# Kernel optimization log

Hardware: AMD Instinct MI355X
Metric: run time of the kernel (lower is better)

Reference implementation:

```python
import jax, jax.numpy as jnp
import numpy as np

N_NODES = 50000


def _add_self_loops(edge_index, num_nodes):
    loop = jnp.arange(num_nodes, dtype=edge_index.dtype)
    src = jnp.concatenate([edge_index[0], loop])
    dst = jnp.concatenate([edge_index[1], loop])
    return src, dst


def _gcn_norm(src, dst, num_nodes, dtype):
    # symmetric normalization: deg^{-1/2}[src] * deg^{-1/2}[dst]
    deg = jax.ops.segment_sum(jnp.ones_like(dst, dtype=dtype), dst,
                              num_segments=num_nodes)
    dinv = jnp.where(deg > 0, jax.lax.rsqrt(deg), 0.0).astype(dtype)
    return dinv[src] * dinv[dst]


def _gcn_conv(x, src, dst, norm, W, b, num_nodes):
    h = x @ W                                  # [N, out]
    msg = norm[:, None] * h[src]               # [E', out] gather
    agg = jax.ops.segment_sum(msg, dst, num_segments=num_nodes)  # scatter-add
    return agg + b


def setup_inputs() -> dict:
    key = jax.random.key(0)
    k1, k2, k3, k4 = jax.random.split(key, 4)
    x = jax.random.normal(k1, (N_NODES, 64), dtype=jnp.float32)
    edge_index = jax.random.randint(k2, (2, 800000), 0, N_NODES, dtype=jnp.int64)
    W1 = jax.random.normal(k3, (64, 64), dtype=jnp.float32) * (1.0 / np.sqrt(64))
    b1 = jnp.zeros((64,), dtype=jnp.float32)
    W2 = jax.random.normal(k4, (64, 37), dtype=jnp.float32) * (1.0 / np.sqrt(64))
    b2 = jnp.zeros((37,), dtype=jnp.float32)
    return {"x": x, "edge_index": edge_index, "W1": W1, "b1": b1,
            "W2": W2, "b2": b2}


def reference(x, edge_index, W1, b1, W2, b2):
    n = x.shape[0]
    src, dst = _add_self_loops(edge_index, n)
    norm = _gcn_norm(src, dst, n, x.dtype)
    h = _gcn_conv(x, src, dst, norm, W1, b1, n)
    h = jax.nn.relu(h)
    out = _gcn_conv(h, src, dst, norm, W2, b2, n)
    return out
```

## Files before the change

### kernel.cpp

```cpp
#include <hip/hip_runtime.h>
#include <hip/hip_fp16.h>

#define F_OUT 37
#define BSHIFT 7
#define BSIZE 128
#define CAP 3072
#define STAGE_CAP 6144
#define XS_STRIDE 68

__device__ __forceinline__ short4 pack4(float a, float b, float c, float d) {
    union { __half2 h2[2]; short4 s; } u;
    u.h2[0] = __floats2half2_rn(a, b);
    u.h2[1] = __floats2half2_rn(c, d);
    return u.s;
}
__device__ __forceinline__ float4 unpack4(short4 v) {
    union { short4 s; __half2 h2[2]; } u;
    u.s = v;
    float2 lo = __half22float2(u.h2[0]);
    float2 hi = __half22float2(u.h2[1]);
    return make_float4(lo.x, lo.y, hi.x, hi.y);
}


__global__ __launch_bounds__(256) void bucketA(const int* __restrict__ src,
                                               const int* __restrict__ dst,
                                               int E, int C, int nb,
                                               int* __restrict__ gcur,
                                               unsigned* __restrict__ bedge) {
    __shared__ unsigned stage[STAGE_CAP];
    __shared__ int lcnt[400];
    __shared__ int lbase[400];
    int t = threadIdx.x;
    int e0 = blockIdx.x * C;
    int cnt = E - e0; if (cnt > C) cnt = C; if (cnt <= 0) return;

    for (int i = t; i < nb; i += 256) lcnt[i] = 0;
    __syncthreads();
    for (int i = t; i < cnt; i += 256) {
        int s = src[e0 + i], d = dst[e0 + i];
        int b = d >> BSHIFT;
        atomicAdd(&lcnt[b], 1);
        stage[i] = ((unsigned)b << 23) | ((unsigned)(d & (BSIZE - 1)) << 16) | (unsigned)s;
    }
    __syncthreads();
    for (int i = t; i < nb; i += 256)
        lbase[i] = lcnt[i] ? atomicAdd(&gcur[i * 16], lcnt[i]) : 0;
    __syncthreads();
    for (int i = t; i < nb; i += 256) lcnt[i] = 0;
    __syncthreads();
    for (int i = t; i < cnt; i += 256) {
        unsigned w = stage[i];
        int b = w >> 23;
        int pos = b * CAP + lbase[b] + atomicAdd(&lcnt[b], 1);
        bedge[pos] = w & 0x7FFFFFu;
    }
}

__global__ __launch_bounds__(256) void bucketB(const unsigned* __restrict__ bedge,
                                               const int* __restrict__ gcur,
                                               int n,
                                               int* __restrict__ rowbeg,
                                               int* __restrict__ rowend,
                                               int* __restrict__ srcIdx,
                                               float* __restrict__ dinv) {
    __shared__ int hcnt[BSIZE], hoff[BSIZE], hcur[BSIZE], tmp[BSIZE];
    int b = blockIdx.x;
    int t = threadIdx.x;
    int cntb = gcur[b * 16];
    int base = b * CAP;
    const unsigned* ed = bedge + (size_t)base;

    if (t < BSIZE) { hcnt[t] = 0; hcur[t] = 0; }
    __syncthreads();
    for (int i = t; i < cntb; i += 256) atomicAdd(&hcnt[ed[i] >> 16], 1);
    __syncthreads();
    if (t < BSIZE) tmp[t] = hcnt[t];
    __syncthreads();
    for (int o = 1; o < BSIZE; o <<= 1) {
        int a = (t < BSIZE && t >= o) ? tmp[t - o] : 0;
        __syncthreads();
        if (t < BSIZE) tmp[t] += a;
        __syncthreads();
    }
    if (t < BSIZE) hoff[t] = tmp[t] - hcnt[t];
    __syncthreads();
    int node = b * BSIZE + t;
    if (t < BSIZE && node < n) {
        rowbeg[node] = base + hoff[t];
        rowend[node] = base + hoff[t] + hcnt[t];
        dinv[node] = rsqrtf(1.0f + (float)hcnt[t]);
    }
    for (int i = t; i < cntb; i += 256) {
        unsigned w = ed[i];
        int dloc = w >> 16;
        int pos = base + hoff[dloc] + atomicAdd(&hcur[dloc], 1);
        srcIdx[pos] = (int)(w & 0xFFFFu);
    }
}


#define MICRO_STEP(XI, ACC)                                                    \
    do {                                                                       \
        ACC[0] += XI.x * w0.x; ACC[1] += XI.x * w0.y;                          \
        ACC[2] += XI.x * w0.z; ACC[3] += XI.x * w0.w;                          \
        ACC[0] += XI.y * w1.x; ACC[1] += XI.y * w1.y;                          \
        ACC[2] += XI.y * w1.z; ACC[3] += XI.y * w1.w;                          \
        ACC[0] += XI.z * w2.x; ACC[1] += XI.z * w2.y;                          \
        ACC[2] += XI.z * w2.z; ACC[3] += XI.z * w2.w;                          \
        ACC[0] += XI.w * w3.x; ACC[1] += XI.w * w3.y;                          \
        ACC[2] += XI.w * w3.z; ACC[3] += XI.w * w3.w;                          \
    } while (0)

__global__ __launch_bounds__(256, 4) void gemm64(const float* __restrict__ x,
                                                 const float* __restrict__ W,
                                                 const float* __restrict__ dinv,
                                                 short4* __restrict__ hsv, int n) {
    __shared__ float Xs[64 * XS_STRIDE];
    __shared__ float Ws[64 * 64];
    int t = threadIdx.x;
    const float4* W4 = (const float4*)W;
#pragma unroll
    for (int i = 0; i < 4; ++i)
        ((float4*)Ws)[t + i * 256] = W4[t + i * 256];
    int row0 = blockIdx.x * 64;
#pragma unroll
    for (int i = 0; i < 4; ++i) {
        int idx = i * 256 + t;
        int r = idx >> 4, k4 = idx & 15;
        int grow = row0 + r;
        float4 v = (grow < n) ? ((const float4*)x)[(size_t)grow * 16 + k4]
                              : make_float4(0.f, 0.f, 0.f, 0.f);
        *(float4*)&Xs[r * XS_STRIDE + k4 * 4] = v;
    }
    __syncthreads();

    int tc = t & 15, tr = t >> 4;
    float a0[4] = {0.f, 0.f, 0.f, 0.f};
    float a1[4] = {0.f, 0.f, 0.f, 0.f};
    float a2[4] = {0.f, 0.f, 0.f, 0.f};
    float a3[4] = {0.f, 0.f, 0.f, 0.f};

#pragma unroll 2
    for (int k = 0; k < 64; k += 4) {
        float4 w0 = *(const float4*)&Ws[(k + 0) * 64 + 4 * tc];
        float4 w1 = *(const float4*)&Ws[(k + 1) * 64 + 4 * tc];
        float4 w2 = *(const float4*)&Ws[(k + 2) * 64 + 4 * tc];
        float4 w3 = *(const float4*)&Ws[(k + 3) * 64 + 4 * tc];
        float4 x0 = *(const float4*)&Xs[(4 * tr + 0) * XS_STRIDE + k];
        float4 x1 = *(const float4*)&Xs[(4 * tr + 1) * XS_STRIDE + k];
        float4 x2 = *(const float4*)&Xs[(4 * tr + 2) * XS_STRIDE + k];
        float4 x3 = *(const float4*)&Xs[(4 * tr + 3) * XS_STRIDE + k];
        MICRO_STEP(x0, a0);
        MICRO_STEP(x1, a1);
        MICRO_STEP(x2, a2);
        MICRO_STEP(x3, a3);
    }

#define STORE64(ACC, R)                                                        \
    do {                                                                       \
        int row = row0 + 4 * tr + (R);                                         \
        if (row < n) {                                                         \
            float dd = dinv[row];                                              \
            hsv[(size_t)row * 16 + tc] =                                       \
                pack4(ACC[0] * dd, ACC[1] * dd, ACC[2] * dd, ACC[3] * dd);     \
        }                                                                      \
    } while (0)
    STORE64(a0, 0); STORE64(a1, 1); STORE64(a2, 2); STORE64(a3, 3);
#undef STORE64
}

__global__ __launch_bounds__(256, 4) void gemm37(const short4* __restrict__ h1v,
                                                 const float* __restrict__ W,
                                                 short4* __restrict__ g32v,
                                                 short4* __restrict__ g8v, int n) {
    __shared__ float Xs[64 * XS_STRIDE];
    __shared__ float Ws[64 * 64];
    int t = threadIdx.x;
    for (int i = t; i < 64 * 64; i += 256) {
        int k = i >> 6, c = i & 63;
        Ws[i] = (c < F_OUT) ? W[k * F_OUT + c] : 0.f;
    }
    int row0 = blockIdx.x * 64;
#pragma unroll
    for (int i = 0; i < 4; ++i) {
        int idx = i * 256 + t;
        int r = idx >> 4, k4 = idx & 15;
        int grow = row0 + r;
        float4 v = (grow < n) ? unpack4(h1v[(size_t)grow * 16 + k4])
                              : make_float4(0.f, 0.f, 0.f, 0.f);
        *(float4*)&Xs[r * XS_STRIDE + k4 * 4] = v;
    }
    __syncthreads();

    int tc = t & 15, tr = t >> 4;
    float a0[4] = {0.f, 0.f, 0.f, 0.f};
    float a1[4] = {0.f, 0.f, 0.f, 0.f};
    float a2[4] = {0.f, 0.f, 0.f, 0.f};
    float a3[4] = {0.f, 0.f, 0.f, 0.f};

#pragma unroll 2
    for (int k = 0; k < 64; k += 4) {
        float4 w0 = *(const float4*)&Ws[(k + 0) * 64 + 4 * tc];
        float4 w1 = *(const float4*)&Ws[(k + 1) * 64 + 4 * tc];
        float4 w2 = *(const float4*)&Ws[(k + 2) * 64 + 4 * tc];
        float4 w3 = *(const float4*)&Ws[(k + 3) * 64 + 4 * tc];
        float4 x0 = *(const float4*)&Xs[(4 * tr + 0) * XS_STRIDE + k];
        float4 x1 = *(const float4*)&Xs[(4 * tr + 1) * XS_STRIDE + k];
        float4 x2 = *(const float4*)&Xs[(4 * tr + 2) * XS_STRIDE + k];
        float4 x3 = *(const float4*)&Xs[(4 * tr + 3) * XS_STRIDE + k];
        MICRO_STEP(x0, a0);
        MICRO_STEP(x1, a1);
        MICRO_STEP(x2, a2);
        MICRO_STEP(x3, a3);
    }

    if (tc < 10) {
#define STORE37(ACC, R)                                                        \
        do {                                                                   \
            int row = row0 + 4 * tr + (R);                                     \
            if (row < n) {                                                     \
                short4 pv = pack4(ACC[0], ACC[1], ACC[2], ACC[3]);             \
                if (tc < 8) g32v[(size_t)row * 8 + tc] = pv;                   \
                else        g8v[(size_t)row * 2 + (tc - 8)] = pv;              \
            }                                                                  \
        } while (0)
        STORE37(a0, 0); STORE37(a1, 1); STORE37(a2, 2); STORE37(a3, 3);
#undef STORE37
    }
}


#define ACCP4(A, B, C, D)                                                      \
    acc.x += (A.x + B.x) + (C.x + D.x);                                        \
    acc.y += (A.y + B.y) + (C.y + D.y);                                        \
    acc.z += (A.z + B.z) + (C.z + D.z);                                        \
    acc.w += (A.w + B.w) + (C.w + D.w);

__global__ void agg64_kernel(const int* __restrict__ rowbeg,
                             const int* __restrict__ rowend,
                             const int* __restrict__ srcIdx,
                             const float* __restrict__ dinv,
                             const short4* __restrict__ hsv,
                             const float* __restrict__ bias,
                             short4* __restrict__ outv, int n) {
    int t = blockIdx.x * blockDim.x + threadIdx.x;
    int d = t >> 4, sub = t & 15;
    if (d >= n) return;
    int gbase = threadIdx.x & 48;
    float4 acc = unpack4(hsv[(size_t)d * 16 + sub]);
    int beg = rowbeg[d], end = rowend[d];
    int j = beg;
#define LD64(Q) float4 v##Q = unpack4(hsv[(size_t)__shfl(myIdx, gbase + Q) * 16 + sub]);
    for (; j + 16 <= end; j += 16) {
        int myIdx = srcIdx[j + sub];
        LD64(0) LD64(1) LD64(2) LD64(3) LD64(4) LD64(5) LD64(6) LD64(7)
        LD64(8) LD64(9) LD64(10) LD64(11) LD64(12) LD64(13) LD64(14) LD64(15)
        ACCP4(v0, v1, v2, v3) ACCP4(v4, v5, v6, v7)
        ACCP4(v8, v9, v10, v11) ACCP4(v12, v13, v14, v15)
    }
    if (j + 8 <= end) {
        int myIdx = srcIdx[j + sub];
        LD64(0) LD64(1) LD64(2) LD64(3) LD64(4) LD64(5) LD64(6) LD64(7)
        ACCP4(v0, v1, v2, v3) ACCP4(v4, v5, v6, v7)
        j += 8;
    }
    if (j + 4 <= end) {
        int s0 = srcIdx[j], s1 = srcIdx[j + 1], s2 = srcIdx[j + 2], s3 = srcIdx[j + 3];
        float4 v0 = unpack4(hsv[(size_t)s0 * 16 + sub]);
        float4 v1 = unpack4(hsv[(size_t)s1 * 16 + sub]);
        float4 v2 = unpack4(hsv[(size_t)s2 * 16 + sub]);
        float4 v3 = unpack4(hsv[(size_t)s3 * 16 + sub]);
        ACCP4(v0, v1, v2, v3)
        j += 4;
    }
    for (; j < end; ++j) {
        float4 v = unpack4(hsv[(size_t)srcIdx[j] * 16 + sub]);
        acc.x += v.x; acc.y += v.y; acc.z += v.z; acc.w += v.w;
    }
#undef LD64
    float dd = dinv[d];
    float4 b = ((const float4*)bias)[sub];
    outv[(size_t)d * 16 + sub] =
        pack4(fmaxf(acc.x * dd + b.x, 0.f) * dd,
              fmaxf(acc.y * dd + b.y, 0.f) * dd,
              fmaxf(acc.z * dd + b.z, 0.f) * dd,
              fmaxf(acc.w * dd + b.w, 0.f) * dd);
}

__global__ void agg40_kernel(const int* __restrict__ rowbeg,
                             const int* __restrict__ rowend,
                             const int* __restrict__ srcIdx,
                             const float* __restrict__ dinv,
                             const short4* __restrict__ g32v,
                             const short4* __restrict__ g8v,
                             const float* __restrict__ bias,
                             float* __restrict__ out, int n) {
    int t = blockIdx.x * blockDim.x + threadIdx.x;
    int d = t >> 4, sub = t & 15;
    if (d >= n) return;
    int gbase = threadIdx.x & 48;
    bool act = sub < 10;
    const short4* tab = (sub < 8) ? (g32v + sub) : (g8v + (sub - 8));
    size_t stride = (sub < 8) ? 8 : 2;
    float4 acc = make_float4(0.f, 0.f, 0.f, 0.f);
    if (act) acc = unpack4(tab[(size_t)d * stride]);
    int beg = rowbeg[d], end = rowend[d];
    int j = beg;
#define SH40(Q) int s##Q = __shfl(myIdx, gbase + Q);
#define G40(Q)  float4 v##Q = unpack4(tab[(size_t)s##Q * stride]);
    for (; j + 16 <= end; j += 16) {
        int myIdx = srcIdx[j + sub];
        SH40(0) SH40(1) SH40(2) SH40(3) SH40(4) SH40(5) SH40(6) SH40(7)
        SH40(8) SH40(9) SH40(10) SH40(11) SH40(12) SH40(13) SH40(14) SH40(15)
        if (act) {
            G40(0) G40(1) G40(2) G40(3) G40(4) G40(5) G40(6) G40(7)
            G40(8) G40(9) G40(10) G40(11) G40(12) G40(13) G40(14) G40(15)
            ACCP4(v0, v1, v2, v3) ACCP4(v4, v5, v6, v7)
            ACCP4(v8, v9, v10, v11) ACCP4(v12, v13, v14, v15)
        }
    }
    if (j + 8 <= end) {
        int myIdx = srcIdx[j + sub];
        SH40(0) SH40(1) SH40(2) SH40(3) SH40(4) SH40(5) SH40(6) SH40(7)
        if (act) {
            G40(0) G40(1) G40(2) G40(3) G40(4) G40(5) G40(6) G40(7)
            ACCP4(v0, v1, v2, v3) ACCP4(v4, v5, v6, v7)
        }
        j += 8;
    }
    if (j + 4 <= end) {
        int s0 = srcIdx[j], s1 = srcIdx[j + 1], s2 = srcIdx[j + 2], s3 = srcIdx[j + 3];
        if (act) {
            float4 v0 = unpack4(tab[(size_t)s0 * stride]);
            float4 v1 = unpack4(tab[(size_t)s1 * stride]);
            float4 v2 = unpack4(tab[(size_t)s2 * stride]);
            float4 v3 = unpack4(tab[(size_t)s3 * stride]);
            ACCP4(v0, v1, v2, v3)
        }
        j += 4;
    }
    for (; j < end; ++j) {
        int s = srcIdx[j];
        if (act) {
            float4 v = unpack4(tab[(size_t)s * stride]);
            acc.x += v.x; acc.y += v.y; acc.z += v.z; acc.w += v.w;
        }
    }
#undef SH40
#undef G40
    if (act) {
        float dd = dinv[d];
        int c0 = 4 * sub;
        float* o = &out[(size_t)d * F_OUT + c0];
        o[0] = acc.x * dd + bias[c0];
        if (c0 + 1 < F_OUT) o[1] = acc.y * dd + bias[c0 + 1];
        if (c0 + 2 < F_OUT) o[2] = acc.z * dd + bias[c0 + 2];
        if (c0 + 3 < F_OUT) o[3] = acc.w * dd + bias[c0 + 3];
    }
}

extern "C" void kernel_launch(void* const* d_in, const int* in_sizes, int n_in,
                              void* d_out, int out_size, void* d_ws, size_t ws_size,
                              hipStream_t stream) {
    const float* x  = (const float*)d_in[0];
    const int*   ei = (const int*)d_in[1];
    const float* W1 = (const float*)d_in[2];
    const float* b1 = (const float*)d_in[3];
    const float* W2 = (const float*)d_in[4];
    const float* b2 = (const float*)d_in[5];
    float* out = (float*)d_out;

    const int n = in_sizes[0] / 64;
    const int E = in_sizes[1] / 2;
    const int* src = ei;
    const int* dst = ei + E;

    const int nb = (n + BSIZE - 1) >> BSHIFT;
    const int nblkA = (E + STAGE_CAP - 1) / STAGE_CAP;
    const int C = (E + nblkA - 1) / nblkA;

    char* p = (char*)d_ws;
    int*   gcur   = (int*)p;   p += (size_t)nb * 16 * 4;
    int*   rowbeg = (int*)p;   p += (size_t)(n + 4) * 4;
    int*   rowend = (int*)p;   p += (size_t)(n + 4) * 4;
    float* dinv   = (float*)p; p += (size_t)n * 4;
    int*   srcIdx = (int*)p;   p += ((size_t)nb * CAP + 16) * 4;
    short4* hsv   = (short4*)p; p += (size_t)n * 64 * 2;
    short4* h1v   = (short4*)p; p += (size_t)n * 64 * 2;
    unsigned* bedge = (unsigned*)hsv;
    short4* g32v  = hsv;
    short4* g8v   = hsv + (size_t)n * 8;

    hipMemsetAsync(gcur, 0, (size_t)nb * 16 * 4, stream);
    bucketA<<<nblkA, 256, 0, stream>>>(src, dst, E, C, nb, gcur, bedge);
    bucketB<<<nb, 256, 0, stream>>>(bedge, gcur, n, rowbeg, rowend, srcIdx, dinv);

    const int gemmBlocks = (n + 63) / 64;
    const int aggBlocks  = (n * 16 + 255) / 256;

    gemm64<<<gemmBlocks, 256, 0, stream>>>(x, W1, dinv, hsv, n);
    agg64_kernel<<<aggBlocks, 256, 0, stream>>>(rowbeg, rowend, srcIdx, dinv, hsv, b1, h1v, n);

    gemm37<<<gemmBlocks, 256, 0, stream>>>(h1v, W2, g32v, g8v, n);
    agg40_kernel<<<aggBlocks, 256, 0, stream>>>(rowbeg, rowend, srcIdx, dinv, g32v, g8v, b2, out, n);
}
```

Baseline: 110.8 us.

## Split layer-1 features into two 32-column halves aggregated in separate passes

Result: slower. 126.7 us (+14.3%).

```diff
diff --git a/kernel.cpp b/kernel.cpp
--- a/kernel.cpp
+++ b/kernel.cpp
@@ -20,6 +20,11 @@
     float2 lo = __half22float2(u.h2[0]);
     float2 hi = __half22float2(u.h2[1]);
     return make_float4(lo.x, lo.y, hi.x, hi.y);
+}
+__device__ __forceinline__ void nt_store_s4(short4 v, short4* p) {
+    union { short4 s; unsigned long long u; } cv;
+    cv.s = v;
+    __builtin_nontemporal_store(cv.u, (unsigned long long*)p);
 }
 
 
@@ -115,7 +120,8 @@
 __global__ __launch_bounds__(256, 4) void gemm64(const float* __restrict__ x,
                                                  const float* __restrict__ W,
                                                  const float* __restrict__ dinv,
-                                                 short4* __restrict__ hsv, int n) {
+                                                 short4* __restrict__ hv0,
+                                                 short4* __restrict__ hv1, int n) {
     __shared__ float Xs[64 * XS_STRIDE];
     __shared__ float Ws[64 * 64];
     int t = threadIdx.x;
@@ -157,12 +163,14 @@
         MICRO_STEP(x3, a3);
     }
 
+    short4* tab = (tc < 8) ? hv0 : hv1;
+    int lc = tc & 7;
 #define STORE64(ACC, R)                                                        \
     do {                                                                       \
         int row = row0 + 4 * tr + (R);                                         \
         if (row < n) {                                                         \
             float dd = dinv[row];                                              \
-            hsv[(size_t)row * 16 + tc] =                                       \
+            tab[(size_t)row * 8 + lc] =                                        \
                 pack4(ACC[0] * dd, ACC[1] * dd, ACC[2] * dd, ACC[3] * dd);     \
         }                                                                      \
     } while (0)
@@ -170,7 +178,8 @@
 #undef STORE64
 }
 
-__global__ __launch_bounds__(256, 4) void gemm37(const short4* __restrict__ h1v,
+__global__ __launch_bounds__(256, 4) void gemm37(const short4* __restrict__ h1v0,
+                                                 const short4* __restrict__ h1v1,
                                                  const float* __restrict__ W,
                                                  short4* __restrict__ g32v,
                                                  short4* __restrict__ g8v, int n) {
@@ -187,8 +196,10 @@
         int idx = i * 256 + t;
         int r = idx >> 4, k4 = idx & 15;
         int grow = row0 + r;
-        float4 v = (grow < n) ? unpack4(h1v[(size_t)grow * 16 + k4])
-                              : make_float4(0.f, 0.f, 0.f, 0.f);
+        float4 v = make_float4(0.f, 0.f, 0.f, 0.f);
+        if (grow < n)
+            v = unpack4((k4 < 8) ? h1v0[(size_t)grow * 8 + k4]
+                                 : h1v1[(size_t)grow * 8 + (k4 - 8)]);
         *(float4*)&Xs[r * XS_STRIDE + k4 * 4] = v;
     }
     __syncthreads();
@@ -237,55 +248,60 @@
     acc.z += (A.z + B.z) + (C.z + D.z);                                        \
     acc.w += (A.w + B.w) + (C.w + D.w);
 
-__global__ void agg64_kernel(const int* __restrict__ rowbeg,
-                             const int* __restrict__ rowend,
-                             const int* __restrict__ srcIdx,
-                             const float* __restrict__ dinv,
-                             const short4* __restrict__ hsv,
-                             const float* __restrict__ bias,
-                             short4* __restrict__ outv, int n) {
+__global__ void agg64s(const int* __restrict__ rowbeg,
+                       const int* __restrict__ rowend,
+                       const int* __restrict__ srcIdx,
+                       const float* __restrict__ dinv,
+                       const short4* __restrict__ tab,
+                       const float* __restrict__ bias,
+                       short4* __restrict__ outv, int n) {
     int t = blockIdx.x * blockDim.x + threadIdx.x;
-    int d = t >> 4, sub = t & 15;
+    int d = t >> 3, sub = t & 7;
     if (d >= n) return;
-    int gbase = threadIdx.x & 48;
-    float4 acc = unpack4(hsv[(size_t)d * 16 + sub]);
-    int beg = rowbeg[d], end = rowend[d];
+    int gbase = threadIdx.x & 56;
+
+    float4 acc = unpack4(tab[(size_t)d * 8 + sub]);
+    int beg = __builtin_nontemporal_load(&rowbeg[d]);
+    int end = __builtin_nontemporal_load(&rowend[d]);
     int j = beg;
-#define LD64(Q) float4 v##Q = unpack4(hsv[(size_t)__shfl(myIdx, gbase + Q) * 16 + sub]);
+#define LDA8(Q) float4 va##Q = unpack4(tab[(size_t)__shfl(idxA, gbase + Q) * 8 + sub]);
+#define LDB8(Q) float4 vb##Q = unpack4(tab[(size_t)__shfl(idxB, gbase + Q) * 8 + sub]);
     for (; j + 16 <= end; j += 16) {
-        int myIdx = srcIdx[j + sub];
-        LD64(0) LD64(1) LD64(2) LD64(3) LD64(4) LD64(5) LD64(6) LD64(7)
-        LD64(8) LD64(9) LD64(10) LD64(11) LD64(12) LD64(13) LD64(14) LD64(15)
-        ACCP4(v0, v1, v2, v3) ACCP4(v4, v5, v6, v7)
-        ACCP4(v8, v9, v10, v11) ACCP4(v12, v13, v14, v15)
+        int idxA = __builtin_nontemporal_load(&srcIdx[j + sub]);
+        int idxB = __builtin_nontemporal_load(&srcIdx[j + 8 + sub]);
+        LDA8(0) LDA8(1) LDA8(2) LDA8(3) LDA8(4) LDA8(5) LDA8(6) LDA8(7)
+        LDB8(0) LDB8(1) LDB8(2) LDB8(3) LDB8(4) LDB8(5) LDB8(6) LDB8(7)
+        ACCP4(va0, va1, va2, va3) ACCP4(va4, va5, va6, va7)
+        ACCP4(vb0, vb1, vb2, vb3) ACCP4(vb4, vb5, vb6, vb7)
     }
     if (j + 8 <= end) {
-        int myIdx = srcIdx[j + sub];
-        LD64(0) LD64(1) LD64(2) LD64(3) LD64(4) LD64(5) LD64(6) LD64(7)
-        ACCP4(v0, v1, v2, v3) ACCP4(v4, v5, v6, v7)
+        int idxA = __builtin_nontemporal_load(&srcIdx[j + sub]);
+        LDA8(0) LDA8(1) LDA8(2) LDA8(3) LDA8(4) LDA8(5) LDA8(6) LDA8(7)
+        ACCP4(va0, va1, va2, va3) ACCP4(va4, va5, va6, va7)
         j += 8;
     }
     if (j + 4 <= end) {
         int s0 = srcIdx[j], s1 = srcIdx[j + 1], s2 = srcIdx[j + 2], s3 = srcIdx[j + 3];
-        float4 v0 = unpack4(hsv[(size_t)s0 * 16 + sub]);
-        float4 v1 = unpack4(hsv[(size_t)s1 * 16 + sub]);
-        float4 v2 = unpack4(hsv[(size_t)s2 * 16 + sub]);
-        float4 v3 = unpack4(hsv[(size_t)s3 * 16 + sub]);
+        float4 v0 = unpack4(tab[(size_t)s0 * 8 + sub]);
+        float4 v1 = unpack4(tab[(size_t)s1 * 8 + sub]);
+        float4 v2 = unpack4(tab[(size_t)s2 * 8 + sub]);
+        float4 v3 = unpack4(tab[(size_t)s3 * 8 + sub]);
         ACCP4(v0, v1, v2, v3)
         j += 4;
     }
     for (; j < end; ++j) {
-        float4 v = unpack4(hsv[(size_t)srcIdx[j] * 16 + sub]);
+        float4 v = unpack4(tab[(size_t)srcIdx[j] * 8 + sub]);
         acc.x += v.x; acc.y += v.y; acc.z += v.z; acc.w += v.w;
     }
-#undef LD64
+#undef LDA8
+#undef LDB8
     float dd = dinv[d];
     float4 b = ((const float4*)bias)[sub];
-    outv[(size_t)d * 16 + sub] =
-        pack4(fmaxf(acc.x * dd + b.x, 0.f) * dd,
-              fmaxf(acc.y * dd + b.y, 0.f) * dd,
-              fmaxf(acc.z * dd + b.z, 0.f) * dd,
-              fmaxf(acc.w * dd + b.w, 0.f) * dd);
+    short4 pv = pack4(fmaxf(acc.x * dd + b.x, 0.f) * dd,
+                      fmaxf(acc.y * dd + b.y, 0.f) * dd,
+                      fmaxf(acc.z * dd + b.z, 0.f) * dd,
+                      fmaxf(acc.w * dd + b.w, 0.f) * dd);
+    nt_store_s4(pv, &outv[(size_t)d * 8 + sub]);
 }
 
 __global__ void agg40_kernel(const int* __restrict__ rowbeg,
@@ -305,12 +321,13 @@
     size_t stride = (sub < 8) ? 8 : 2;
     float4 acc = make_float4(0.f, 0.f, 0.f, 0.f);
     if (act) acc = unpack4(tab[(size_t)d * stride]);
-    int beg = rowbeg[d], end = rowend[d];
+    int beg = __builtin_nontemporal_load(&rowbeg[d]);
+    int end = __builtin_nontemporal_load(&rowend[d]);
     int j = beg;
 #define SH40(Q) int s##Q = __shfl(myIdx, gbase + Q);
 #define G40(Q)  float4 v##Q = unpack4(tab[(size_t)s##Q * stride]);
     for (; j + 16 <= end; j += 16) {
-        int myIdx = srcIdx[j + sub];
+        int myIdx = __builtin_nontemporal_load(&srcIdx[j + sub]);
         SH40(0) SH40(1) SH40(2) SH40(3) SH40(4) SH40(5) SH40(6) SH40(7)
         SH40(8) SH40(9) SH40(10) SH40(11) SH40(12) SH40(13) SH40(14) SH40(15)
         if (act) {
@@ -321,7 +338,7 @@
         }
     }
     if (j + 8 <= end) {
-        int myIdx = srcIdx[j + sub];
+        int myIdx = __builtin_nontemporal_load(&srcIdx[j + sub]);
         SH40(0) SH40(1) SH40(2) SH40(3) SH40(4) SH40(5) SH40(6) SH40(7)
         if (act) {
             G40(0) G40(1) G40(2) G40(3) G40(4) G40(5) G40(6) G40(7)
@@ -353,10 +370,10 @@
         float dd = dinv[d];
         int c0 = 4 * sub;
         float* o = &out[(size_t)d * F_OUT + c0];
-        o[0] = acc.x * dd + bias[c0];
-        if (c0 + 1 < F_OUT) o[1] = acc.y * dd + bias[c0 + 1];
-        if (c0 + 2 < F_OUT) o[2] = acc.z * dd + bias[c0 + 2];
-        if (c0 + 3 < F_OUT) o[3] = acc.w * dd + bias[c0 + 3];
+        __builtin_nontemporal_store(acc.x * dd + bias[c0], &o[0]);
+        if (c0 + 1 < F_OUT) __builtin_nontemporal_store(acc.y * dd + bias[c0 + 1], &o[1]);
+        if (c0 + 2 < F_OUT) __builtin_nontemporal_store(acc.z * dd + bias[c0 + 2], &o[2]);
+        if (c0 + 3 < F_OUT) __builtin_nontemporal_store(acc.w * dd + bias[c0 + 3], &o[3]);
     }
 }
 
@@ -386,22 +403,26 @@
     int*   rowend = (int*)p;   p += (size_t)(n + 4) * 4;
     float* dinv   = (float*)p; p += (size_t)n * 4;
     int*   srcIdx = (int*)p;   p += ((size_t)nb * CAP + 16) * 4;
-    short4* hsv   = (short4*)p; p += (size_t)n * 64 * 2;
-    short4* h1v   = (short4*)p; p += (size_t)n * 64 * 2;
-    unsigned* bedge = (unsigned*)hsv;
-    short4* g32v  = hsv;
-    short4* g8v   = hsv + (size_t)n * 8;
+    short4* hv0   = (short4*)p; p += (size_t)n * 32 * 2;
+    short4* hv1   = (short4*)p; p += (size_t)n * 32 * 2;
+    short4* h1v0  = (short4*)p; p += (size_t)n * 32 * 2;
+    short4* h1v1  = (short4*)p; p += (size_t)n * 32 * 2;
+    unsigned* bedge = (unsigned*)hv0;
+    short4* g32v  = hv0;
+    short4* g8v   = hv1;
 
     hipMemsetAsync(gcur, 0, (size_t)nb * 16 * 4, stream);
     bucketA<<<nblkA, 256, 0, stream>>>(src, dst, E, C, nb, gcur, bedge);
     bucketB<<<nb, 256, 0, stream>>>(bedge, gcur, n, rowbeg, rowend, srcIdx, dinv);
 
     const int gemmBlocks = (n + 63) / 64;
-    const int aggBlocks  = (n * 16 + 255) / 256;
-
-    gemm64<<<gemmBlocks, 256, 0, stream>>>(x, W1, dinv, hsv, n);
-    agg64_kernel<<<aggBlocks, 256, 0, stream>>>(rowbeg, rowend, srcIdx, dinv, hsv, b1, h1v, n);
-
-    gemm37<<<gemmBlocks, 256, 0, stream>>>(h1v, W2, g32v, g8v, n);
-    agg40_kernel<<<aggBlocks, 256, 0, stream>>>(rowbeg, rowend, srcIdx, dinv, g32v, g8v, b2, out, n);
-}
+    const int aggS   = (n * 8 + 255) / 256;
+    const int agg16  = (n * 16 + 255) / 256;
+
+    gemm64<<<gemmBlocks, 256, 0, stream>>>(x, W1, dinv, hv0, hv1, n);
+    agg64s<<<aggS, 256, 0, stream>>>(rowbeg, rowend, srcIdx, dinv, hv0, b1,      h1v0, n);
+    agg64s<<<aggS, 256, 0, stream>>>(rowbeg, rowend, srcIdx, dinv, hv1, b1 + 32, h1v1, n);
+
+    gemm37<<<gemmBlocks, 256, 0, stream>>>(h1v0, h1v1, W2, g32v, g8v, n);
+    agg40_kernel<<<agg16, 256, 0, stream>>>(rowbeg, rowend, srcIdx, dinv, g32v, g8v, b2, out, n);
+}
```
